# Kernel tuning notes

Hardware: AMD Instinct MI355X
Metric: run time of the kernel (lower is better)

Reference implementation:

```python
import jax, jax.numpy as jnp
import numpy as np

DG = 8   # deformable groups
K = 3    # DCNv2 kernel size


def conv1x1(x, w):
    return jnp.einsum('bhwc,cf->bhwf', x, w)


def conv3x3_same(x, w, b):
    out = jax.lax.conv_general_dilated(x, w, (1, 1), 'SAME',
                                       dimension_numbers=('NHWC', 'HWIO', 'NHWC'))
    return out + b


def dcn_v2(x, offset, mask, weight, bias):
    # x: [B,H,W,C]; offset: [B,H,W,DG,K*K,2] (dy,dx); mask: [B,H,W,DG,K*K]
    B, H, W, C = x.shape
    cpg = C // DG
    ky, kx = jnp.meshgrid(jnp.arange(K) - (K // 2), jnp.arange(K) - (K // 2), indexing='ij')
    ky = ky.reshape(-1).astype(x.dtype)  # [K*K]
    kx = kx.reshape(-1).astype(x.dtype)
    iy = jnp.arange(H, dtype=x.dtype)[None, :, None, None, None]
    ix = jnp.arange(W, dtype=x.dtype)[None, None, :, None, None]
    yp = iy + ky + offset[..., 0]   # [B,H,W,DG,KK] sample rows
    xp = ix + kx + offset[..., 1]   # sample cols

    # group-major flattened feature map for gather: [B,DG,H*W,cpg]
    xt = jnp.transpose(x.reshape(B, H, W, DG, cpg), (0, 3, 1, 2, 4)).reshape(B, DG, H * W, cpg)

    def gather(yi, xi):
        valid = ((yi >= 0) & (yi < H) & (xi >= 0) & (xi < W)).astype(x.dtype)
        yc = jnp.clip(yi, 0, H - 1)
        xc = jnp.clip(xi, 0, W - 1)
        flat = (yc * W + xc).astype(jnp.int32)               # [B,H,W,DG,KK]
        idx = jnp.transpose(flat, (0, 3, 1, 2, 4)).reshape(B, DG, -1)
        v = jnp.take_along_axis(xt, idx[..., None], axis=2)  # [B,DG,H*W*KK,cpg]
        v = v.reshape(B, DG, H, W, K * K, cpg)
        v = jnp.transpose(v, (0, 2, 3, 1, 4, 5))             # [B,H,W,DG,KK,cpg]
        return v * valid[..., None]

    y0 = jnp.floor(yp); x0 = jnp.floor(xp)
    wy = (yp - y0)[..., None]; wx = (xp - x0)[..., None]
    val = (gather(y0, x0) * (1 - wy) * (1 - wx)
           + gather(y0, x0 + 1) * (1 - wy) * wx
           + gather(y0 + 1, x0) * wy * (1 - wx)
           + gather(y0 + 1, x0 + 1) * wy * wx)
    val = val * mask[..., None]                               # modulated sampling
    # [B,H,W,DG,KK,cpg] -> [B,H,W,KK,C] (global channel = g*cpg + r)
    val = jnp.transpose(val, (0, 1, 2, 4, 3, 5)).reshape(B, H, W, K * K, C)
    out = jnp.einsum('bhwkc,kcf->bhwf', val, weight.reshape(K * K, C, -1))
    return out + bias


def setup_inputs() -> dict:
    key = jax.random.key(0)
    ks = jax.random.split(key, 8)
    B, H, W, Cf, Cc, F = 4, 64, 64, 256, 256, 256
    fine = jax.random.normal(ks[0], (B, H, W, Cf), jnp.float32)
    coarse = jax.random.normal(ks[1], (B, H // 2, W // 2, Cc), jnp.float32)
    attend_w = jax.random.normal(ks[2], (Cf, Cf), jnp.float32) * 0.05
    select_w = jax.random.normal(ks[3], (Cf, F), jnp.float32) * 0.05
    offset_w = jax.random.normal(ks[4], (F + Cc, 2 * F), jnp.float32) * 0.05
    om_w = jax.random.normal(ks[5], (3, 3, 2 * F, DG * 3 * K * K), jnp.float32) * 0.01
    om_b = jnp.zeros((DG * 3 * K * K,), jnp.float32)
    dcn_w = jax.random.normal(ks[6], (3, 3, Cc, F), jnp.float32) * 0.05
    dcn_b = jnp.zeros((F,), jnp.float32)
    return {'fine': fine, 'coarse': coarse, 'attend_w': attend_w, 'select_w': select_w,
            'offset_w': offset_w, 'om_w': om_w, 'om_b': om_b, 'dcn_w': dcn_w, 'dcn_b': dcn_b}


def reference(fine, coarse, attend_w, select_w, offset_w, om_w, om_b, dcn_w, dcn_b):
    B, H, W, Cf = fine.shape
    Cc = coarse.shape[-1]
    # BilinearInterpolation: upsample coarse to fine resolution
    coarse_up = jax.image.resize(coarse, (B, H, W, Cc), 'bilinear')
    # FeatureSelection: GAP -> 1x1 sigmoid attention, residual gate, 1x1 proj
    attn = jax.nn.sigmoid(conv1x1(jnp.mean(fine, axis=(1, 2), keepdims=True), attend_w))
    fine_cal = conv1x1(fine * (attn + 1.0), select_w)
    # offset features from concat(selected fine, 2*coarse)
    align = conv1x1(jnp.concatenate([fine_cal, coarse_up * 2.0], axis=-1), offset_w)
    # DCNv2 internal offset/mask conv (3x3) on alignment features
    om = conv3x3_same(align, om_w, om_b)          # [B,H,W,DG*3*K*K]
    n_off = DG * 2 * K * K
    off = om[..., :n_off].reshape(B, H, W, DG, K * K, 2)
    mask = jax.nn.sigmoid(om[..., n_off:]).reshape(B, H, W, DG, K * K)
    aligned = dcn_v2(coarse_up, off, mask, dcn_w, dcn_b)
    return jax.nn.relu(aligned) + fine_cal
```

## Files before the change

### kernel.cpp

```cpp
#include <hip/hip_runtime.h>
#include <math.h>


typedef __attribute__((ext_vector_type(8))) short bf16x8;
typedef __attribute__((ext_vector_type(4))) short bf16x4;
typedef __attribute__((ext_vector_type(4))) float f32x4;
#define MFMA16(a,b,c) __builtin_amdgcn_mfma_f32_16x16x32_bf16(a,b,c,0,0,0)

__device__ inline short f2b(float x){
  union { float f; unsigned u; } v; v.f = x;
  unsigned r = v.u + 0x7FFFu + ((v.u >> 16) & 1u);
  return (short)(r >> 16);
}
__device__ inline float b2f(short s){
  union { unsigned u; float f; } v;
  v.u = ((unsigned)(unsigned short)s) << 16;
  return v.f;
}

#define OFS_GATE  1024u
#define OFS_PART  2048u
#define OFS_CUPB  264192u
#define OFS_FCAL  4458496u
#define OFS_ALGB  8652800u
#define OFS_OM    12847104u
#define OFS_DWB   16386048u
#define OFS_OMWB  16680960u
#define OFS_SWB   17270784u
#define OFS_OWB   17401856u

__global__ __launch_bounds__(256) void k_gap(const float* __restrict__ fine,
                                             float* __restrict__ part){
  __shared__ float red[4*256];
  int b = blockIdx.x >> 6, chunk = blockIdx.x & 63;
  int c4 = threadIdx.x & 63, rl = threadIdx.x >> 6;
  const float4* F4 = (const float4*)fine;
  float4 s = {0.f,0.f,0.f,0.f};
  for (int it = 0; it < 16; ++it){
    int row = chunk*64 + it*4 + rl;
    float4 v = F4[((size_t)(b*4096 + row))*64 + c4];
    s.x += v.x; s.y += v.y; s.z += v.z; s.w += v.w;
  }
  *(float4*)&red[rl*256 + c4*4] = s;
  __syncthreads();
  int c = threadIdx.x;
  part[(size_t)blockIdx.x*256 + c] = red[c] + red[256+c] + red[512+c] + red[768+c];
}

__global__ __launch_bounds__(256) void k_misc(const float* __restrict__ part,
                                              const float* __restrict__ aw,
                                              float* __restrict__ gate,
                                              const float* __restrict__ dw,
                                              const float* __restrict__ omw,
                                              const float* __restrict__ ow,
                                              const float* __restrict__ sw,
                                              short* __restrict__ dwb,
                                              short* __restrict__ omwb,
                                              short* __restrict__ owb,
                                              short* __restrict__ swb,
                                              const float* __restrict__ coarse,
                                              short* __restrict__ cupb){
  int blk = blockIdx.x;
  if (blk < 4){
    __shared__ float m[256];
    int b = blk, f = threadIdx.x;
    float sm = 0.f;
    for (int ch = 0; ch < 64; ++ch) sm += part[(size_t)(b*64 + ch)*256 + f];
    m[f] = sm * (1.f/4096.f);
    __syncthreads();
    float s = 0.f;
    for (int c = 0; c < 256; ++c) s += m[c] * aw[c*256 + f];
    gate[b*256 + f] = 1.f + 1.f/(1.f + expf(-s));
  } else if (blk < 292){
    int t = (blk - 4)*256 + threadIdx.x;
    int l = t & 63, nt = (t >> 6) & 15, ksg = t >> 10;
    int n = nt*16 + (l & 15);
    int kb = ksg*32 + (l >> 4)*8;
    bf16x8 o;
#pragma unroll
    for (int j = 0; j < 8; ++j) o[j] = f2b(dw[(size_t)(kb + j)*256 + n]);
    ((bf16x8*)dwb)[t] = o;
  } else if (blk < 868){
    int t = (blk - 292)*256 + threadIdx.x;
    int l = t & 63, nt = (t >> 6) & 15, ksg = t >> 10;
    int n = nt*16 + (l & 15);
    int kb = ksg*32 + (l >> 4)*8;
    bf16x8 o;
#pragma unroll
    for (int j = 0; j < 8; ++j)
      o[j] = (n < 216) ? f2b(omw[(size_t)(kb + j)*216 + n]) : (short)0;
    ((bf16x8*)omwb)[t] = o;
  } else if (blk < 996){
    int t = (blk - 868)*256 + threadIdx.x;
    int l = t & 63, nt = (t >> 6) & 31, ksg = t >> 11;
    int n = nt*16 + (l & 15);
    int kb = ksg*32 + (l >> 4)*8;
    float sc = (kb >= 256) ? 2.f : 1.f;
    bf16x8 o;
#pragma unroll
    for (int j = 0; j < 8; ++j) o[j] = f2b(sc * ow[(size_t)(kb + j)*512 + n]);
    ((bf16x8*)owb)[t] = o;
  } else if (blk < 1124){
    int t = (blk - 996)*256 + threadIdx.x;
    int l = t & 63, nt = (t >> 6) & 15, ksg = t >> 10;
    int n = nt*16 + (l & 15);
    int kb = ksg*32 + (l >> 4)*8;
    bf16x8 o;
#pragma unroll
    for (int j = 0; j < 8; ++j) o[j] = f2b(sw[(size_t)(kb + j)*256 + n]);
    ((bf16x8*)swb)[t] = o;
  } else {
    int idx = (blk - 1124)*256 + threadIdx.x;
    int c4 = idx & 63, x = (idx >> 6) & 63, y = (idx >> 12) & 63, b = idx >> 18;
    float fy = 0.5f*y - 0.25f, fx = 0.5f*x - 0.25f;
    float yf = floorf(fy), xf = floorf(fx);
    float wy = fy - yf, wx = fx - xf;
    int r0 = max(0, min(31, (int)yf)), r1 = max(0, min(31, (int)yf + 1));
    int c0 = max(0, min(31, (int)xf)), c1 = max(0, min(31, (int)xf + 1));
    const float4* src = (const float4*)coarse;
    float4 v00 = src[((b*32 + r0)*32 + c0)*64 + c4];
    float4 v01 = src[((b*32 + r0)*32 + c1)*64 + c4];
    float4 v10 = src[((b*32 + r1)*32 + c0)*64 + c4];
    float4 v11 = src[((b*32 + r1)*32 + c1)*64 + c4];
    float w00 = (1.f-wy)*(1.f-wx), w01 = (1.f-wy)*wx, w10 = wy*(1.f-wx), w11 = wy*wx;
    bf16x4 o = { f2b(v00.x*w00 + v01.x*w01 + v10.x*w10 + v11.x*w11),
                 f2b(v00.y*w00 + v01.y*w01 + v10.y*w10 + v11.y*w11),
                 f2b(v00.z*w00 + v01.z*w01 + v10.z*w10 + v11.z*w11),
                 f2b(v00.w*w00 + v01.w*w01 + v10.w*w10 + v11.w*w11) };
    ((bf16x4*)cupb)[idx] = o;
  }
}

#define FST 264
__global__ __launch_bounds__(256) void k_fa(const float* __restrict__ fine,
                                            const float* __restrict__ gate,
                                            const short* __restrict__ swb,
                                            const short* __restrict__ owb,
                                            const short* __restrict__ cupb,
                                            float* __restrict__ fcal,
                                            short* __restrict__ algb){
  __shared__ float g4[256];
  __shared__ short ab[32*FST];
  int m0 = blockIdx.x*32, b = m0 >> 12;
  int tid = threadIdx.x, lane = tid & 63, wave = tid >> 6;
  int arow = lane & 15, aquad = lane >> 4;
  g4[tid] = gate[b*256 + tid];
  __syncthreads();
  const float4* F4 = (const float4*)(fine + (size_t)m0*256);
  const float4* G4 = (const float4*)g4;
  for (int it = 0; it < 8; ++it){
    int idx = it*256 + tid;
    int row = idx >> 6, c4 = idx & 63;
    float4 v = F4[row*64 + c4];
    float4 gg = G4[c4];
    bf16x4 s4 = { f2b(v.x*gg.x), f2b(v.y*gg.y), f2b(v.z*gg.z), f2b(v.w*gg.w) };
    *(bf16x4*)&ab[row*FST + c4*4] = s4;
  }
  __syncthreads();
  f32x4 acc[2][4];
#pragma unroll
  for (int s = 0; s < 2; ++s)
#pragma unroll
    for (int t = 0; t < 4; ++t) acc[s][t] = (f32x4){0.f,0.f,0.f,0.f};
  const bf16x8* W8 = (const bf16x8*)swb;
  for (int ks = 0; ks < 8; ++ks){
    bf16x8 a0 = *(const bf16x8*)&ab[arow*FST + ks*32 + aquad*8];
    bf16x8 a1 = *(const bf16x8*)&ab[(16 + arow)*FST + ks*32 + aquad*8];
    const bf16x8* wp = W8 + ((size_t)(ks*16 + wave*4))*64 + lane;
#pragma unroll
    for (int t = 0; t < 4; ++t){
      bf16x8 bw = wp[t*64];
      acc[0][t] = MFMA16(a0, bw, acc[0][t]);
      acc[1][t] = MFMA16(a1, bw, acc[1][t]);
    }
  }
  __syncthreads();
#pragma unroll
  for (int t = 0; t < 4; ++t){
    int f = wave*64 + t*16 + arow;
#pragma unroll
    for (int s = 0; s < 2; ++s)
#pragma unroll
      for (int r = 0; r < 4; ++r){
        int mloc = s*16 + aquad*4 + r;
        float v = acc[s][t][r];
        fcal[(size_t)(m0 + mloc)*256 + f] = v;
        ab[mloc*FST + f] = f2b(v);
      }
  }
  __syncthreads();
  f32x4 acc2[2][8];
#pragma unroll
  for (int s = 0; s < 2; ++s)
#pragma unroll
    for (int t = 0; t < 8; ++t) acc2[s][t] = (f32x4){0.f,0.f,0.f,0.f};
  const bf16x8* OW8 = (const bf16x8*)owb;
  for (int ks = 0; ks < 16; ++ks){
    bf16x8 a0, a1;
    if (ks < 8){
      a0 = *(const bf16x8*)&ab[arow*FST + ks*32 + aquad*8];
      a1 = *(const bf16x8*)&ab[(16 + arow)*FST + ks*32 + aquad*8];
    } else {
      int ko = (ks - 8)*32 + aquad*8;
      a0 = *(const bf16x8*)(cupb + (size_t)(m0 + arow)*256 + ko);
      a1 = *(const bf16x8*)(cupb + (size_t)(m0 + 16 + arow)*256 + ko);
    }
    const bf16x8* wp = OW8 + ((size_t)(ks*32 + wave*8))*64 + lane;
#pragma unroll
    for (int t = 0; t < 8; ++t){
      bf16x8 bw = wp[t*64];
      acc2[0][t] = MFMA16(a0, bw, acc2[0][t]);
      acc2[1][t] = MFMA16(a1, bw, acc2[1][t]);
    }
  }
#pragma unroll
  for (int t = 0; t < 8; ++t){
    int n = wave*128 + t*16 + arow;
#pragma unroll
    for (int s = 0; s < 2; ++s)
#pragma unroll
      for (int r = 0; r < 4; ++r){
        int m = m0 + s*16 + aquad*4 + r;
        algb[(size_t)m*512 + n] = f2b(acc2[s][t][r]);
      }
  }
}

#define XST 520
__global__ __launch_bounds__(256) void k_om(const short* __restrict__ algb,
                                            const short* __restrict__ omwb,
                                            const float* __restrict__ omb,
                                            float* __restrict__ om){
  __shared__ short xbuf[34*XST];
  int blk = blockIdx.x;
  int m0 = (blk >> 1)*32, nh = blk & 1;
  int b = m0 >> 12, y = (m0 & 4095) >> 6, x0 = m0 & 63;
  int tid = threadIdx.x;
  int lane = tid & 63, wave = tid >> 6;
  int arow = lane & 15, aquad = lane >> 4;
  f32x4 acc[2][2];
#pragma unroll
  for (int s = 0; s < 2; ++s)
#pragma unroll
    for (int t = 0; t < 2; ++t) acc[s][t] = (f32x4){0.f,0.f,0.f,0.f};
  const bf16x8* W8 = (const bf16x8*)omwb;
  for (int ky = 0; ky < 3; ++ky){
    int yy = y + ky - 1;
    if ((unsigned)yy >= 64u) continue;
    __syncthreads();
    const short* srow = algb + (size_t)((b*64 + yy)*64)*512;
    for (int it = 0; it < 9; ++it){
      int idx = it*256 + tid;
      if (idx < 2176){
        int xx = idx >> 6, l8 = idx & 63;
        int gx = x0 - 1 + xx;
        bf16x8 v = (bf16x8){0,0,0,0,0,0,0,0};
        if ((unsigned)gx < 64u) v = *(const bf16x8*)(srow + (size_t)gx*512 + l8*8);
        *(bf16x8*)&xbuf[xx*XST + l8*8] = v;
      }
    }
    __syncthreads();
    for (int ks = 0; ks < 48; ++ks){
      int kl = ks*32 + aquad*8;
      int kx = kl >> 9, cc = kl & 511;
      bf16x8 a0 = *(const bf16x8*)&xbuf[(arow + kx)*XST + cc];
      bf16x8 a1 = *(const bf16x8*)&xbuf[(16 + arow + kx)*XST + cc];
      const bf16x8* wp = W8 + ((size_t)((ky*48 + ks)*16 + nh*8 + wave*2))*64 + lane;
#pragma unroll
      for (int t = 0; t < 2; ++t){
        bf16x8 bw = wp[t*64];
        acc[0][t] = MFMA16(a0, bw, acc[0][t]);
        acc[1][t] = MFMA16(a1, bw, acc[1][t]);
      }
    }
  }
#pragma unroll
  for (int t = 0; t < 2; ++t){
    int f = nh*128 + wave*32 + t*16 + arow;
    if (f < 216){
      float bias = omb[f];
      bool is_mask = (f >= 144);
#pragma unroll
      for (int s = 0; s < 2; ++s)
#pragma unroll
        for (int r = 0; r < 4; ++r){
          int m = m0 + s*16 + aquad*4 + r;
          float v = acc[s][t][r] + bias;
          if (is_mask) v = 1.f/(1.f + expf(-v));
          om[(size_t)m*216 + f] = v;
        }
    }
  }
}

#define VST 776
__global__ __launch_bounds__(512) void k_dcn(const short* __restrict__ cupb,
                                             const float* __restrict__ om,
                                             const short* __restrict__ dwb,
                                             const float* __restrict__ db,
                                             const float* __restrict__ fcal,
                                             float* __restrict__ out){
  __shared__ short valb[32*VST];
  int bid = ((blockIdx.x & 7) << 6) | (blockIdx.x >> 3);
  int m0 = bid*32;
  int b = m0 >> 12, y = (m0 & 4095) >> 6, x0 = m0 & 63;
  int tid = threadIdx.x;
  int lane = tid & 63, wave = tid >> 6;
  int unit = tid >> 2, lane4 = tid & 3;
  int arow = lane & 15, aquad = lane >> 4;
  f32x4 acc[2][2];
#pragma unroll
  for (int s = 0; s < 2; ++s)
#pragma unroll
    for (int t = 0; t < 2; ++t) acc[s][t] = (f32x4){0.f,0.f,0.f,0.f};
  const short* cpb = cupb + (size_t)b*4096*256;
  const bf16x8* W8 = (const bf16x8*)dwb;

  for (int ph = 0; ph < 3; ++ph){
    __syncthreads();
    for (int it = 0; it < 6; ++it){
      int u = it*128 + unit;
      int i = u / 24; int r = u - i*24; int g = r / 3; int kk = r - g*3;
      const float* omp = om + (size_t)(m0 + i)*216;
      int k = ph*3 + kk;
      float dy = omp[(g*9 + k)*2 + 0];
      float dx = omp[(g*9 + k)*2 + 1];
      float mv = omp[144 + g*9 + k];
      float yp = (float)(y + ph - 1) + dy;
      float xp = (float)(x0 + i + kk - 1) + dx;
      float yf = floorf(yp), xf = floorf(xp);
      float wy = yp - yf, wx = xp - xf;
      int iy = (int)yf, ix = (int)xf;
      float wA = (1.f-wy)*(1.f-wx), wB = (1.f-wy)*wx, wC = wy*(1.f-wx), wD = wy*wx;
      bool y0ok = (unsigned)iy < 64u, y1ok = (unsigned)(iy+1) < 64u;
      bool x0ok = (unsigned)ix < 64u, x1ok = (unsigned)(ix+1) < 64u;
      if (!(y0ok && x0ok)) wA = 0.f;
      if (!(y0ok && x1ok)) wB = 0.f;
      if (!(y1ok && x0ok)) wC = 0.f;
      if (!(y1ok && x1ok)) wD = 0.f;
      int y0c = min(max(iy, 0), 63), y1c = min(max(iy + 1, 0), 63);
      int x0c = min(max(ix, 0), 63), x1c = min(max(ix + 1, 0), 63);
      int cofs = g*32 + lane4*8;
      bf16x8 l00 = *(const bf16x8*)(cpb + (size_t)(y0c*64 + x0c)*256 + cofs);
      bf16x8 l01 = *(const bf16x8*)(cpb + (size_t)(y0c*64 + x1c)*256 + cofs);
      bf16x8 l10 = *(const bf16x8*)(cpb + (size_t)(y1c*64 + x0c)*256 + cofs);
      bf16x8 l11 = *(const bf16x8*)(cpb + (size_t)(y1c*64 + x1c)*256 + cofs);
      bf16x8 o;
#pragma unroll
      for (int j = 0; j < 8; ++j){
        float v = wA*b2f(l00[j]) + wB*b2f(l01[j]) + wC*b2f(l10[j]) + wD*b2f(l11[j]);
        o[j] = f2b(v * mv);
      }
      *(bf16x8*)&valb[i*VST + kk*256 + g*32 + lane4*8] = o;
    }
    __syncthreads();
    for (int ks = 0; ks < 24; ++ks){
      bf16x8 a0 = *(const bf16x8*)&valb[arow*VST + ks*32 + aquad*8];
      bf16x8 a1 = *(const bf16x8*)&valb[(16 + arow)*VST + ks*32 + aquad*8];
      const bf16x8* wp = W8 + ((size_t)((ph*24 + ks)*16 + wave*2))*64 + lane;
#pragma unroll
      for (int t = 0; t < 2; ++t){
        bf16x8 bw = wp[t*64];
        acc[0][t] = MFMA16(a0, bw, acc[0][t]);
        acc[1][t] = MFMA16(a1, bw, acc[1][t]);
      }
    }
  }
#pragma unroll
  for (int t = 0; t < 2; ++t){
    int f = wave*32 + t*16 + (lane & 15);
    float bias = db[f];
#pragma unroll
    for (int s = 0; s < 2; ++s)
#pragma unroll
      for (int r = 0; r < 4; ++r){
        int m = m0 + s*16 + aquad*4 + r;
        out[(size_t)m*256 + f] = fmaxf(acc[s][t][r] + bias, 0.f) + fcal[(size_t)m*256 + f];
      }
  }
}

extern "C" void kernel_launch(void* const* d_in, const int* in_sizes, int n_in,
                              void* d_out, int out_size, void* d_ws, size_t ws_size,
                              hipStream_t stream){
  const float* fine     = (const float*)d_in[0];
  const float* coarse   = (const float*)d_in[1];
  const float* attend_w = (const float*)d_in[2];
  const float* select_w = (const float*)d_in[3];
  const float* offset_w = (const float*)d_in[4];
  const float* om_w     = (const float*)d_in[5];
  const float* om_b     = (const float*)d_in[6];
  const float* dcn_w    = (const float*)d_in[7];
  const float* dcn_b    = (const float*)d_in[8];
  float* out = (float*)d_out;
  float* ws  = (float*)d_ws;

  float* gate = ws + OFS_GATE;
  float* part = ws + OFS_PART;
  short* cupb = (short*)(ws + OFS_CUPB);
  float* fcal = ws + OFS_FCAL;
  short* algb = (short*)(ws + OFS_ALGB);
  float* om   = ws + OFS_OM;
  short* dwb  = (short*)(ws + OFS_DWB);
  short* omwb = (short*)(ws + OFS_OMWB);
  short* swb  = (short*)(ws + OFS_SWB);
  short* owb  = (short*)(ws + OFS_OWB);

  hipLaunchKernelGGL(k_gap,  dim3(256),  dim3(256), 0, stream, fine, part);
  hipLaunchKernelGGL(k_misc, dim3(5220), dim3(256), 0, stream, part, attend_w, gate,
                     dcn_w, om_w, offset_w, select_w, dwb, omwb, owb, swb, coarse, cupb);
  hipLaunchKernelGGL(k_fa,   dim3(512),  dim3(256), 0, stream, fine, gate, swb, owb,
                     cupb, fcal, algb);
  hipLaunchKernelGGL(k_om,   dim3(1024), dim3(256), 0, stream, algb, omwb, om_b, om);
  hipLaunchKernelGGL(k_dcn,  dim3(512),  dim3(512), 0, stream, cupb, om, dwb, dcn_b, fcal, out);
  (void)in_sizes; (void)n_in; (void)out_size; (void)ws_size;
}
```

Before: 254.3 us.

## Retile 3x3 offset conv to full-row 64-pixel tiles with all output channels per block

The k_om 3x3 conv now processes a whole image row of 64 pixels and all 256 output channels per block with 8 waves. Each wave reuses four A fragments per weight load. Previously two blocks split the output channels and re-read the same input halo. Input staging is split into two 256-channel halves so the shared buffer stays moderate. Blocks are also remapped (XCD-style swizzle) so that neighboring rows run on different dies. This cuts redundant activation loads and raises MFMA work per weight fetch, at the cost of fewer blocks (256), more accumulator registers, and extra syncs per channel half.

```diff
diff --git a/kernel.cpp b/kernel.cpp
--- a/kernel.cpp
+++ b/kernel.cpp
@@ -226,66 +226,74 @@
   }
 }
 
-#define XST 520
-__global__ __launch_bounds__(256) void k_om(const short* __restrict__ algb,
+#define XST2 264
+__global__ __launch_bounds__(512) void k_om(const short* __restrict__ algb,
                                             const short* __restrict__ omwb,
                                             const float* __restrict__ omb,
                                             float* __restrict__ om){
-  __shared__ short xbuf[34*XST];
-  int blk = blockIdx.x;
-  int m0 = (blk >> 1)*32, nh = blk & 1;
-  int b = m0 >> 12, y = (m0 & 4095) >> 6, x0 = m0 & 63;
+  __shared__ short xbuf[66*XST2];
+  int blk = ((blockIdx.x & 7) << 5) | (blockIdx.x >> 3);
+  int m0 = blk*64;
+  int b = m0 >> 12, y = (m0 >> 6) & 63;
   int tid = threadIdx.x;
   int lane = tid & 63, wave = tid >> 6;
   int arow = lane & 15, aquad = lane >> 4;
-  f32x4 acc[2][2];
-#pragma unroll
-  for (int s = 0; s < 2; ++s)
-#pragma unroll
-    for (int t = 0; t < 2; ++t) acc[s][t] = (f32x4){0.f,0.f,0.f,0.f};
+  f32x4 acc[4][2];
+#pragma unroll
+  for (int mi = 0; mi < 4; ++mi)
+#pragma unroll
+    for (int t = 0; t < 2; ++t) acc[mi][t] = (f32x4){0.f,0.f,0.f,0.f};
   const bf16x8* W8 = (const bf16x8*)omwb;
   for (int ky = 0; ky < 3; ++ky){
     int yy = y + ky - 1;
     if ((unsigned)yy >= 64u) continue;
-    __syncthreads();
     const short* srow = algb + (size_t)((b*64 + yy)*64)*512;
-    for (int it = 0; it < 9; ++it){
-      int idx = it*256 + tid;
-      if (idx < 2176){
-        int xx = idx >> 6, l8 = idx & 63;
-        int gx = x0 - 1 + xx;
-        bf16x8 v = (bf16x8){0,0,0,0,0,0,0,0};
-        if ((unsigned)gx < 64u) v = *(const bf16x8*)(srow + (size_t)gx*512 + l8*8);
-        *(bf16x8*)&xbuf[xx*XST + l8*8] = v;
-      }
-    }
-    __syncthreads();
-    for (int ks = 0; ks < 48; ++ks){
-      int kl = ks*32 + aquad*8;
-      int kx = kl >> 9, cc = kl & 511;
-      bf16x8 a0 = *(const bf16x8*)&xbuf[(arow + kx)*XST + cc];
-      bf16x8 a1 = *(const bf16x8*)&xbuf[(16 + arow + kx)*XST + cc];
-      const bf16x8* wp = W8 + ((size_t)((ky*48 + ks)*16 + nh*8 + wave*2))*64 + lane;
-#pragma unroll
-      for (int t = 0; t < 2; ++t){
-        bf16x8 bw = wp[t*64];
-        acc[0][t] = MFMA16(a0, bw, acc[0][t]);
-        acc[1][t] = MFMA16(a1, bw, acc[1][t]);
+    for (int h = 0; h < 2; ++h){
+      __syncthreads();
+      for (int it = 0; it < 5; ++it){
+        int u = it*512 + tid;
+        if (u < 2112){
+          int xx = u >> 5, cu = u & 31;
+          int gx = xx - 1;
+          bf16x8 v = (bf16x8){0,0,0,0,0,0,0,0};
+          if ((unsigned)gx < 64u)
+            v = *(const bf16x8*)(srow + (size_t)gx*512 + h*256 + cu*8);
+          *(bf16x8*)&xbuf[xx*XST2 + cu*8] = v;
+        }
+      }
+      __syncthreads();
+#pragma unroll
+      for (int kx = 0; kx < 3; ++kx){
+        for (int s = 0; s < 8; ++s){
+          int w48 = kx*16 + h*8 + s;
+          bf16x8 a[4];
+#pragma unroll
+          for (int mi = 0; mi < 4; ++mi)
+            a[mi] = *(const bf16x8*)&xbuf[(mi*16 + arow + kx)*XST2 + s*32 + aquad*8];
+          const bf16x8* wp = W8 + ((size_t)((ky*48 + w48)*16 + wave*2))*64 + lane;
+#pragma unroll
+          for (int t = 0; t < 2; ++t){
+            bf16x8 bw = wp[t*64];
+#pragma unroll
+            for (int mi = 0; mi < 4; ++mi)
+              acc[mi][t] = MFMA16(a[mi], bw, acc[mi][t]);
+          }
+        }
       }
     }
   }
 #pragma unroll
   for (int t = 0; t < 2; ++t){
-    int f = nh*128 + wave*32 + t*16 + arow;
+    int f = wave*32 + t*16 + arow;
     if (f < 216){
       float bias = omb[f];
       bool is_mask = (f >= 144);
 #pragma unroll
-      for (int s = 0; s < 2; ++s)
+      for (int mi = 0; mi < 4; ++mi)
 #pragma unroll
         for (int r = 0; r < 4; ++r){
-          int m = m0 + s*16 + aquad*4 + r;
-          float v = acc[s][t][r] + bias;
+          int m = m0 + mi*16 + aquad*4 + r;
+          float v = acc[mi][t][r] + bias;
           if (is_mask) v = 1.f/(1.f + expf(-v));
           om[(size_t)m*216 + f] = v;
         }
@@ -411,7 +419,7 @@
                      dcn_w, om_w, offset_w, select_w, dwb, omwb, owb, swb, coarse, cupb);
   hipLaunchKernelGGL(k_fa,   dim3(512),  dim3(256), 0, stream, fine, gate, swb, owb,
                      cupb, fcal, algb);
-  hipLaunchKernelGGL(k_om,   dim3(1024), dim3(256), 0, stream, algb, omwb, om_b, om);
+  hipLaunchKernelGGL(k_om,   dim3(256),  dim3(512), 0, stream, algb, omwb, om_b, om);
   hipLaunchKernelGGL(k_dcn,  dim3(512),  dim3(512), 0, stream, cupb, om, dwb, dcn_b, fcal, out);
   (void)in_sizes; (void)n_in; (void)out_size; (void)ws_size;
 }
```

New measurement: 251.2 us. No clear change (-1.2%).
